# Performance work log

Hardware: AMD Instinct MI355X
Metric: run time of the kernel (lower is better)

Reference implementation:

```python
import jax, jax.numpy as jnp
import numpy as np
from functools import partial

N_NODES = 50000
N_EDGES = 800000
IN_F, HID_F, OUT_F = 128, 128, 64


def _linear_params(key, in_f, out_f):
    k1, k2 = jax.random.split(key)
    bound = 1.0 / np.sqrt(in_f)
    W = jax.random.uniform(k1, (out_f, in_f), jnp.float32, -bound, bound)
    b = jax.random.uniform(k2, (out_f,), jnp.float32, -bound, bound)
    return W, b


def setup_inputs() -> dict:
    key = jax.random.key(0)
    ks = jax.random.split(key, 10)
    features = jax.random.normal(ks[0], (N_NODES, IN_F), jnp.float32)
    src = jax.random.randint(ks[1], (N_EDGES,), 0, N_NODES, jnp.int32)
    dst = jax.random.randint(ks[2], (N_EDGES,), 0, N_NODES, jnp.int32)
    W1a, b1a = _linear_params(ks[3], IN_F, HID_F)
    W1b, b1b = _linear_params(ks[4], HID_F, HID_F)
    W2a, b2a = _linear_params(ks[5], HID_F, HID_F)
    W2b, b2b = _linear_params(ks[6], HID_F, HID_F)
    W3a, b3a = _linear_params(ks[7], HID_F, HID_F)
    W3b, b3b = _linear_params(ks[8], HID_F, OUT_F)
    return dict(features=features, src=src, dst=dst,
                W1a=W1a, b1a=b1a, W1b=W1b, b1b=b1b,
                W2a=W2a, b2a=b2a, W2b=W2b, b2b=b2b,
                W3a=W3a, b3a=b3a, W3b=W3b, b3b=b3b)


def _mean_agg(x, src, dst, n_nodes):
    # gather src features, segment-sum into dst, divide by in-degree (0-deg -> 0)
    summed = jax.ops.segment_sum(x[src], dst, num_segments=n_nodes)
    deg = jax.ops.segment_sum(jnp.ones((src.shape[0],), x.dtype), dst,
                              num_segments=n_nodes)
    return summed / jnp.maximum(deg, 1.0)[:, None]


def _gin_conv(x, src, dst, Wa, ba, Wb, bb):
    # DGL GINConv, aggregator 'mean', eps=0: h = MLP((1+eps)*x + mean_agg)
    h = x + _mean_agg(x, src, dst, x.shape[0])
    h = jax.nn.relu(h @ Wa.T + ba)
    return h @ Wb.T + bb


def reference(features, src, dst,
              W1a, b1a, W1b, b1b,
              W2a, b2a, W2b, b2b,
              W3a, b3a, W3b, b3b):
    x = jax.nn.relu(_gin_conv(features, src, dst, W1a, b1a, W1b, b1b))
    x = jax.nn.relu(_gin_conv(x, src, dst, W2a, b2a, W2b, b2b))
    x = jax.nn.relu(x @ W3a.T + b3a)
    return x @ W3b.T + b3b
```

## Files before the change

kernel.cpp:

```cpp
#include <hip/hip_runtime.h>
#include <hip/hip_fp16.h>

#define N_NODES 50000
#define N_EDGES 800000

typedef __attribute__((ext_vector_type(8))) short bf16x8;
typedef __attribute__((ext_vector_type(4))) float f32x4;

#define OFF_BUFA   0UL
#define OFF_T16    25600000UL
#define OFF_CNT    38400000UL
#define OFF_W      38600064UL
#define OFF_CSR    38960512UL

#define NB_EDGE 3125
#define NB_W    352
#define NB_FEAT 6250

__device__ __forceinline__ unsigned short bf16_rne(float f) {
  unsigned u = __float_as_uint(f);
  unsigned r = (u + 0x7FFFu + ((u >> 16) & 1u)) >> 16;
  return (unsigned short)r;
}

__device__ __forceinline__ int swz(int row, int b) {
  return (row * 256 + b) ^ ((row & 7) << 4);
}

__device__ __forceinline__ void gload_lds16(const void* g, void* l) {
  __builtin_amdgcn_global_load_lds(
      (const __attribute__((address_space(1))) unsigned int*)g,
      (__attribute__((address_space(3))) unsigned int*)l, 16, 0, 0);
}

__global__ __launch_bounds__(256)
void scatter16(const int* __restrict__ src, const int* __restrict__ dst,
               int* __restrict__ cnt, unsigned short* __restrict__ csr) {
  int i = blockIdx.x * 256 + threadIdx.x;
  int d = dst[i];
  int pos = atomicAdd(&cnt[d], 1);
  if (pos < 64) csr[(d << 6) + pos] = (unsigned short)src[i];
}

__global__ __launch_bounds__(256)
void conv_kernel(const float* __restrict__ W1a, const float* __restrict__ W1b,
                 const float* __restrict__ W2a, const float* __restrict__ W2b,
                 const float* __restrict__ W3a, const float* __restrict__ W3b,
                 unsigned short* __restrict__ pool,
                 const float* __restrict__ feat, __half* __restrict__ t16) {
  const int b = blockIdx.x;
  const int tid = threadIdx.x;
  if (b < NB_W) {
    int i = b * 256 + tid;
    const float* s;
    int base, local, msize;
    if (i < 16384)      { s = W1a; base = 0;      local = i;          msize = 16384; }
    else if (i < 32768) { s = W1b; base = 32768;  local = i - 16384;  msize = 16384; }
    else if (i < 49152) { s = W2a; base = 65536;  local = i - 32768;  msize = 16384; }
    else if (i < 65536) { s = W2b; base = 98304;  local = i - 49152;  msize = 16384; }
    else if (i < 81920) { s = W3a; base = 131072; local = i - 65536;  msize = 16384; }
    else                { s = W3b; base = 163840; local = i - 81920;  msize = 8192;  }
    float f = s[local];
    unsigned short hi = bf16_rne(f);
    float fh = __uint_as_float((unsigned)hi << 16);
    pool[base + local] = hi;
    pool[base + msize + local] = bf16_rne(f - fh);
  } else {
    int i = (b - NB_W) * 1024 + tid * 4;
    float4 v = *reinterpret_cast<const float4*>(feat + i);
    ushort4 h;
    h.x = __half_as_ushort(__float2half_rn(v.x));
    h.y = __half_as_ushort(__float2half_rn(v.y));
    h.z = __half_as_ushort(__float2half_rn(v.z));
    h.w = __half_as_ushort(__float2half_rn(v.w));
    *reinterpret_cast<ushort4*>((unsigned short*)t16 + i) = h;
  }
}

template <bool SELF32>
__global__ __launch_bounds__(256)
void agg_kernel(const __half* __restrict__ t16, const float* __restrict__ xself,
                const unsigned short* __restrict__ csr, const int* __restrict__ cnt,
                float* __restrict__ out) {
  int node = blockIdx.x * 4 + (threadIdx.x >> 6);
  if (node >= N_NODES) return;
  const int lane = threadIdx.x & 63;
  int deg = cnt[node];
  int dloop = min(deg, 64);
  int beg = node << 6;
  float inv = 1.0f / fmaxf((float)deg, 1.0f);

  float s0 = 0.f, s1 = 0.f, t0 = 0.f, t1 = 0.f;
  float u0 = 0.f, u1 = 0.f, v0 = 0.f, v1 = 0.f;
  int e = 0;
  for (; e + 3 < dloop; e += 4) {
    ushort4 q = *reinterpret_cast<const ushort4*>(csr + beg + e);
    float2 a = __half22float2(*reinterpret_cast<const __half2*>(t16 + (size_t)q.x * 128 + lane * 2));
    float2 b = __half22float2(*reinterpret_cast<const __half2*>(t16 + (size_t)q.y * 128 + lane * 2));
    float2 c = __half22float2(*reinterpret_cast<const __half2*>(t16 + (size_t)q.z * 128 + lane * 2));
    float2 d = __half22float2(*reinterpret_cast<const __half2*>(t16 + (size_t)q.w * 128 + lane * 2));
    s0 += a.x; s1 += a.y; t0 += b.x; t1 += b.y;
    u0 += c.x; u1 += c.y; v0 += d.x; v1 += d.y;
  }
  for (; e < dloop; ++e) {
    int i0 = csr[beg + e];
    float2 a = __half22float2(*reinterpret_cast<const __half2*>(t16 + (size_t)i0 * 128 + lane * 2));
    s0 += a.x; s1 += a.y;
  }
  float2 sm = make_float2(s0 + t0 + u0 + v0, s1 + t1 + u1 + v1);
  float2 xv;
  if (SELF32) {
    xv = *reinterpret_cast<const float2*>(xself + (size_t)node * 128 + lane * 2);
  } else {
    xv = __half22float2(*reinterpret_cast<const __half2*>(t16 + (size_t)node * 128 + lane * 2));
  }
  float2 o = make_float2(fmaf(sm.x, inv, xv.x), fmaf(sm.y, inv, xv.y));
  *reinterpret_cast<float2*>(out + (size_t)node * 128 + lane * 2) = o;
}

__device__ __forceinline__ void stage_x32(const float* __restrict__ X, int m0, int tid,
                                          char* ahi, char* alo, int M) {
  #pragma unroll
  for (int it = 0; it < 4; ++it) {
    int f = tid + it * 256;
    int row = f >> 5, c = f & 31;
    float4 v = make_float4(0.f, 0.f, 0.f, 0.f);
    if (m0 + row < M)
      v = *reinterpret_cast<const float4*>(X + (size_t)(m0 + row) * 128 + c * 4);
    ushort4 hi, lo;
    float fh;
    hi.x = bf16_rne(v.x); fh = __uint_as_float((unsigned)hi.x << 16); lo.x = bf16_rne(v.x - fh);
    hi.y = bf16_rne(v.y); fh = __uint_as_float((unsigned)hi.y << 16); lo.y = bf16_rne(v.y - fh);
    hi.z = bf16_rne(v.z); fh = __uint_as_float((unsigned)hi.z << 16); lo.z = bf16_rne(v.z - fh);
    hi.w = bf16_rne(v.w); fh = __uint_as_float((unsigned)hi.w << 16); lo.w = bf16_rne(v.w - fh);
    int bo = swz(row, c * 8);
    *reinterpret_cast<ushort4*>(ahi + bo) = hi;
    *reinterpret_cast<ushort4*>(alo + bo) = lo;
  }
}

template <int NR>
__device__ __forceinline__ void stage_w(const unsigned short* __restrict__ gh,
                                        const unsigned short* __restrict__ gl,
                                        char* WH, char* WL, int w, int lane) {
  constexpr int CH = NR / 16;
  #pragma unroll
  for (int k = 0; k < CH; ++k) {
    int base = w * (NR * 64) + k * 1024;
    int ofs = base + lane * 16;
    int row = ofs >> 8;
    int g = ofs ^ ((row & 7) << 4);
    gload_lds16((const char*)gh + g, WH + base);
    gload_lds16((const char*)gl + g, WL + base);
  }
}

template <int NB>
__device__ __forceinline__ void gemm_ll(const char* ahi, const char* alo,
                                        const char* wh, const char* wl,
                                        int w, int lrow, int lg,
                                        f32x4 (&acc)[2][NB]) {
  #pragma unroll
  for (int i = 0; i < 2; ++i)
    #pragma unroll
    for (int nb = 0; nb < NB; ++nb) acc[i][nb] = (f32x4){0.f, 0.f, 0.f, 0.f};
  #pragma unroll
  for (int kk = 0; kk < 4; ++kk) {
    bf16x8 bh[NB], bl[NB];
    #pragma unroll
    for (int nb = 0; nb < NB; ++nb) {
      int col = w * (16 * NB) + nb * 16 + lrow;
      int wo = swz(col, kk * 64 + lg * 16);
      bh[nb] = *reinterpret_cast<const bf16x8*>(wh + wo);
      bl[nb] = *reinterpret_cast<const bf16x8*>(wl + wo);
    }
    #pragma unroll
    for (int i = 0; i < 2; ++i) {
      int bo = swz(i * 16 + lrow, kk * 64 + lg * 16);
      bf16x8 ah = *reinterpret_cast<const bf16x8*>(ahi + bo);
      bf16x8 al = *reinterpret_cast<const bf16x8*>(alo + bo);
      #pragma unroll
      for (int nb = 0; nb < NB; ++nb) {
        acc[i][nb] = __builtin_amdgcn_mfma_f32_16x16x32_bf16(ah, bh[nb], acc[i][nb], 0, 0, 0);
        acc[i][nb] = __builtin_amdgcn_mfma_f32_16x16x32_bf16(al, bh[nb], acc[i][nb], 0, 0, 0);
        acc[i][nb] = __builtin_amdgcn_mfma_f32_16x16x32_bf16(ah, bl[nb], acc[i][nb], 0, 0, 0);
      }
    }
  }
}

__device__ __forceinline__ void store_h32(char* ahi, char* alo, const float* __restrict__ bias,
                                          int w, int lrow, int lg, f32x4 (&acc)[2][2]) {
  #pragma unroll
  for (int i = 0; i < 2; ++i) {
    #pragma unroll
    for (int nb = 0; nb < 2; ++nb) {
      int col = w * 32 + nb * 16 + lrow;
      float b = bias[col];
      #pragma unroll
      for (int r = 0; r < 4; ++r) {
        float v = fmaxf(acc[i][nb][r] + b, 0.f);
        int row = i * 16 + lg * 4 + r;
        unsigned short h = bf16_rne(v);
        float fh = __uint_as_float((unsigned)h << 16);
        unsigned short l2 = bf16_rne(v - fh);
        int bo = swz(row, col * 2);
        *reinterpret_cast<unsigned short*>(ahi + bo) = h;
        *reinterpret_cast<unsigned short*>(alo + bo) = l2;
      }
    }
  }
}

__global__ __launch_bounds__(256)
void mlp1_kernel(const float* __restrict__ X, const unsigned short* __restrict__ p,
                 const float* __restrict__ b1a, const float* __restrict__ b1b,
                 __half* __restrict__ Y, int M) {
  __shared__ __align__(16) unsigned short Ahi[32 * 128];
  __shared__ __align__(16) unsigned short Alo[32 * 128];
  __shared__ __align__(16) unsigned short WHs[128 * 128];
  __shared__ __align__(16) unsigned short WLs[128 * 128];
  char* ahi = (char*)Ahi;
  char* alo = (char*)Alo;
  char* wh = (char*)WHs;
  char* wl = (char*)WLs;
  const int tid = threadIdx.x;
  const int w = tid >> 6, l = tid & 63;
  const int lrow = l & 15, lg = l >> 4;
  const int m0 = blockIdx.x * 32;

  stage_w<128>(p + 0, p + 16384, wh, wl, w, l);
  stage_x32(X, m0, tid, ahi, alo, M);
  __syncthreads();

  f32x4 acc[2][2];
  gemm_ll<2>(ahi, alo, wh, wl, w, lrow, lg, acc);
  __syncthreads();

  stage_w<128>(p + 32768, p + 49152, wh, wl, w, l);
  store_h32(ahi, alo, b1a, w, lrow, lg, acc);
  __syncthreads();

  gemm_ll<2>(ahi, alo, wh, wl, w, lrow, lg, acc);

  #pragma unroll
  for (int i = 0; i < 2; ++i) {
    #pragma unroll
    for (int nb = 0; nb < 2; ++nb) {
      int col = w * 32 + nb * 16 + lrow;
      float b = b1b[col];
      #pragma unroll
      for (int r = 0; r < 4; ++r) {
        float v = fmaxf(acc[i][nb][r] + b, 0.f);
        int row = m0 + i * 16 + lg * 4 + r;
        if (row < M) Y[(size_t)row * 128 + col] = __float2half_rn(v);
      }
    }
  }
}

__global__ __launch_bounds__(256)
void mlp2head_kernel(const float* __restrict__ X, const unsigned short* __restrict__ p,
                     const float* __restrict__ b2a, const float* __restrict__ b2b,
                     const float* __restrict__ b3a, const float* __restrict__ b3b,
                     float* __restrict__ Y, int M) {
  __shared__ __align__(16) unsigned short Ahi[32 * 128];
  __shared__ __align__(16) unsigned short Alo[32 * 128];
  __shared__ __align__(16) unsigned short WHs[128 * 128];
  __shared__ __align__(16) unsigned short WLs[128 * 128];
  char* ahi = (char*)Ahi;
  char* alo = (char*)Alo;
  char* wh = (char*)WHs;
  char* wl = (char*)WLs;
  const int tid = threadIdx.x;
  const int w = tid >> 6, l = tid & 63;
  const int lrow = l & 15, lg = l >> 4;
  const int m0 = blockIdx.x * 32;

  stage_w<128>(p + 65536, p + 81920, wh, wl, w, l);
  stage_x32(X, m0, tid, ahi, alo, M);
  __syncthreads();

  f32x4 acc[2][2];
  gemm_ll<2>(ahi, alo, wh, wl, w, lrow, lg, acc);
  __syncthreads();

  stage_w<128>(p + 98304, p + 114688, wh, wl, w, l);
  store_h32(ahi, alo, b2a, w, lrow, lg, acc);
  __syncthreads();

  gemm_ll<2>(ahi, alo, wh, wl, w, lrow, lg, acc);
  __syncthreads();

  stage_w<128>(p + 131072, p + 147456, wh, wl, w, l);
  store_h32(ahi, alo, b2b, w, lrow, lg, acc);
  __syncthreads();

  gemm_ll<2>(ahi, alo, wh, wl, w, lrow, lg, acc);
  __syncthreads();

  stage_w<64>(p + 163840, p + 172032, wh, wl, w, l);
  store_h32(ahi, alo, b3a, w, lrow, lg, acc);
  __syncthreads();

  f32x4 acc1[2][1];
  gemm_ll<1>(ahi, alo, wh, wl, w, lrow, lg, acc1);

  #pragma unroll
  for (int i = 0; i < 2; ++i) {
    int col = w * 16 + lrow;
    float b = b3b[col];
    #pragma unroll
    for (int r = 0; r < 4; ++r) {
      float v = acc1[i][0][r] + b;
      int row = m0 + i * 16 + lg * 4 + r;
      if (row < M) Y[(size_t)row * 64 + col] = v;
    }
  }
}

extern "C" void kernel_launch(void* const* d_in, const int* in_sizes, int n_in,
                              void* d_out, int out_size, void* d_ws, size_t ws_size,
                              hipStream_t stream) {
  const float* feat = (const float*)d_in[0];
  const int*   esrc = (const int*)d_in[1];
  const int*   edst = (const int*)d_in[2];
  const float* W1a = (const float*)d_in[3];  const float* b1a = (const float*)d_in[4];
  const float* W1b = (const float*)d_in[5];  const float* b1b = (const float*)d_in[6];
  const float* W2a = (const float*)d_in[7];  const float* b2a = (const float*)d_in[8];
  const float* W2b = (const float*)d_in[9];  const float* b2b = (const float*)d_in[10];
  const float* W3a = (const float*)d_in[11]; const float* b3a = (const float*)d_in[12];
  const float* W3b = (const float*)d_in[13]; const float* b3b = (const float*)d_in[14];

  char* ws = (char*)d_ws;
  float*  bufA = (float*)(ws + OFF_BUFA);
  __half* t16  = (__half*)(ws + OFF_T16);
  int*    cnt  = (int*)(ws + OFF_CNT);
  unsigned short* p   = (unsigned short*)(ws + OFF_W);
  unsigned short* csr = (unsigned short*)(ws + OFF_CSR);

  hipMemsetAsync(cnt, 0, 200000, stream);

  scatter16<<<NB_EDGE, 256, 0, stream>>>(esrc, edst, cnt, csr);
  conv_kernel<<<NB_W + NB_FEAT, 256, 0, stream>>>(W1a, W1b, W2a, W2b, W3a, W3b, p, feat, t16);

  const int AB = (N_NODES + 3) / 4;
  const int GB = (N_NODES + 31) / 32;

  agg_kernel<true><<<AB, 256, 0, stream>>>(t16, feat, csr, cnt, bufA);
  mlp1_kernel<<<GB, 256, 0, stream>>>(bufA, p, b1a, b1b, t16, N_NODES);

  agg_kernel<false><<<AB, 256, 0, stream>>>(t16, feat, csr, cnt, bufA);
  mlp2head_kernel<<<GB, 256, 0, stream>>>(bufA, p, b2a, b2b, b3a, b3b,
                                          (float*)d_out, N_NODES);
}
```

Baseline: 211.5 us.

## Retile MLP kernels to 160-row blocks with 512 threads

Both fused MLP kernels move from 32-row tiles on 256 threads to 160-row tiles on 512 threads. Each of the 8 waves now owns a 16-column slice and loops over 10 row sub-tiles, reusing one weight fragment across them. The point is to amortize the per-block staging of the hi/lo bf16 weight matrices over five times as many rows, cutting weight traffic and block count. In exchange the much larger LDS footprint likely allows only one block per CU, and 313 blocks leave an uneven tail across the CUs.

```diff
diff --git a/kernel.cpp b/kernel.cpp
--- a/kernel.cpp
+++ b/kernel.cpp
@@ -16,6 +16,9 @@
 #define NB_EDGE 3125
 #define NB_W    352
 #define NB_FEAT 6250
+
+#define BM 160
+#define GB_MLP 313
 
 __device__ __forceinline__ unsigned short bf16_rne(float f) {
   unsigned u = __float_as_uint(f);
@@ -118,11 +121,11 @@
   *reinterpret_cast<float2*>(out + (size_t)node * 128 + lane * 2) = o;
 }
 
-__device__ __forceinline__ void stage_x32(const float* __restrict__ X, int m0, int tid,
-                                          char* ahi, char* alo, int M) {
-  #pragma unroll
-  for (int it = 0; it < 4; ++it) {
-    int f = tid + it * 256;
+__device__ __forceinline__ void stage_xT(const float* __restrict__ X, int m0, int tid,
+                                         char* ahi, char* alo, int M) {
+  #pragma unroll
+  for (int it = 0; it < 10; ++it) {
+    int f = tid + it * 512;
     int row = f >> 5, c = f & 31;
     float4 v = make_float4(0.f, 0.f, 0.f, 0.f);
     if (m0 + row < M)
@@ -143,10 +146,10 @@
 __device__ __forceinline__ void stage_w(const unsigned short* __restrict__ gh,
                                         const unsigned short* __restrict__ gl,
                                         char* WH, char* WL, int w, int lane) {
-  constexpr int CH = NR / 16;
+  constexpr int CH = NR / 32;
   #pragma unroll
   for (int k = 0; k < CH; ++k) {
-    int base = w * (NR * 64) + k * 1024;
+    int base = w * (NR * 32) + k * 1024;
     int ofs = base + lane * 16;
     int row = ofs >> 8;
     int g = ofs ^ ((row & 7) << 4);
@@ -155,166 +158,146 @@
   }
 }
 
-template <int NB>
-__device__ __forceinline__ void gemm_ll(const char* ahi, const char* alo,
-                                        const char* wh, const char* wl,
-                                        int w, int lrow, int lg,
-                                        f32x4 (&acc)[2][NB]) {
-  #pragma unroll
-  for (int i = 0; i < 2; ++i)
+__device__ __forceinline__ void gemmT(const char* ahi, const char* alo,
+                                      const char* wh, const char* wl,
+                                      int w, int lrow, int lg, f32x4 (&acc)[10]) {
+  #pragma unroll
+  for (int i = 0; i < 10; ++i) acc[i] = (f32x4){0.f, 0.f, 0.f, 0.f};
+  const int col = w * 16 + lrow;
+  #pragma unroll
+  for (int kk = 0; kk < 4; ++kk) {
+    int wo = swz(col, kk * 64 + lg * 16);
+    bf16x8 bh = *reinterpret_cast<const bf16x8*>(wh + wo);
+    bf16x8 bl = *reinterpret_cast<const bf16x8*>(wl + wo);
     #pragma unroll
-    for (int nb = 0; nb < NB; ++nb) acc[i][nb] = (f32x4){0.f, 0.f, 0.f, 0.f};
-  #pragma unroll
-  for (int kk = 0; kk < 4; ++kk) {
-    bf16x8 bh[NB], bl[NB];
-    #pragma unroll
-    for (int nb = 0; nb < NB; ++nb) {
-      int col = w * (16 * NB) + nb * 16 + lrow;
-      int wo = swz(col, kk * 64 + lg * 16);
-      bh[nb] = *reinterpret_cast<const bf16x8*>(wh + wo);
-      bl[nb] = *reinterpret_cast<const bf16x8*>(wl + wo);
-    }
-    #pragma unroll
-    for (int i = 0; i < 2; ++i) {
+    for (int i = 0; i < 10; ++i) {
       int bo = swz(i * 16 + lrow, kk * 64 + lg * 16);
       bf16x8 ah = *reinterpret_cast<const bf16x8*>(ahi + bo);
       bf16x8 al = *reinterpret_cast<const bf16x8*>(alo + bo);
-      #pragma unroll
-      for (int nb = 0; nb < NB; ++nb) {
-        acc[i][nb] = __builtin_amdgcn_mfma_f32_16x16x32_bf16(ah, bh[nb], acc[i][nb], 0, 0, 0);
-        acc[i][nb] = __builtin_amdgcn_mfma_f32_16x16x32_bf16(al, bh[nb], acc[i][nb], 0, 0, 0);
-        acc[i][nb] = __builtin_amdgcn_mfma_f32_16x16x32_bf16(ah, bl[nb], acc[i][nb], 0, 0, 0);
-      }
+      acc[i] = __builtin_amdgcn_mfma_f32_16x16x32_bf16(ah, bh, acc[i], 0, 0, 0);
+      acc[i] = __builtin_amdgcn_mfma_f32_16x16x32_bf16(al, bh, acc[i], 0, 0, 0);
+      acc[i] = __builtin_amdgcn_mfma_f32_16x16x32_bf16(ah, bl, acc[i], 0, 0, 0);
     }
   }
 }
 
-__device__ __forceinline__ void store_h32(char* ahi, char* alo, const float* __restrict__ bias,
-                                          int w, int lrow, int lg, f32x4 (&acc)[2][2]) {
-  #pragma unroll
-  for (int i = 0; i < 2; ++i) {
+__device__ __forceinline__ void store_hT(char* ahi, char* alo, const float* __restrict__ bias,
+                                         int w, int lrow, int lg, f32x4 (&acc)[10]) {
+  const int col = w * 16 + lrow;
+  const float b = bias[col];
+  #pragma unroll
+  for (int i = 0; i < 10; ++i) {
     #pragma unroll
-    for (int nb = 0; nb < 2; ++nb) {
-      int col = w * 32 + nb * 16 + lrow;
-      float b = bias[col];
-      #pragma unroll
-      for (int r = 0; r < 4; ++r) {
-        float v = fmaxf(acc[i][nb][r] + b, 0.f);
-        int row = i * 16 + lg * 4 + r;
-        unsigned short h = bf16_rne(v);
-        float fh = __uint_as_float((unsigned)h << 16);
-        unsigned short l2 = bf16_rne(v - fh);
-        int bo = swz(row, col * 2);
-        *reinterpret_cast<unsigned short*>(ahi + bo) = h;
-        *reinterpret_cast<unsigned short*>(alo + bo) = l2;
-      }
+    for (int r = 0; r < 4; ++r) {
+      float v = fmaxf(acc[i][r] + b, 0.f);
+      int row = i * 16 + lg * 4 + r;
+      unsigned short h = bf16_rne(v);
+      float fh = __uint_as_float((unsigned)h << 16);
+      unsigned short l2 = bf16_rne(v - fh);
+      int bo = swz(row, col * 2);
+      *reinterpret_cast<unsigned short*>(ahi + bo) = h;
+      *reinterpret_cast<unsigned short*>(alo + bo) = l2;
     }
   }
 }
 
-__global__ __launch_bounds__(256)
+__global__ __launch_bounds__(512, 2)
 void mlp1_kernel(const float* __restrict__ X, const unsigned short* __restrict__ p,
                  const float* __restrict__ b1a, const float* __restrict__ b1b,
                  __half* __restrict__ Y, int M) {
-  __shared__ __align__(16) unsigned short Ahi[32 * 128];
-  __shared__ __align__(16) unsigned short Alo[32 * 128];
+  __shared__ __align__(16) unsigned short Ahi[160 * 128];
+  __shared__ __align__(16) unsigned short Alo[160 * 128];
   __shared__ __align__(16) unsigned short WHs[128 * 128];
   __shared__ __align__(16) unsigned short WLs[128 * 128];
-  char* ahi = (char*)Ahi;
-  char* alo = (char*)Alo;
-  char* wh = (char*)WHs;
-  char* wl = (char*)WLs;
+  char* ahi = (char*)Ahi; char* alo = (char*)Alo;
+  char* wh = (char*)WHs;  char* wl = (char*)WLs;
   const int tid = threadIdx.x;
   const int w = tid >> 6, l = tid & 63;
   const int lrow = l & 15, lg = l >> 4;
-  const int m0 = blockIdx.x * 32;
+  const int m0 = blockIdx.x * BM;
 
   stage_w<128>(p + 0, p + 16384, wh, wl, w, l);
-  stage_x32(X, m0, tid, ahi, alo, M);
-  __syncthreads();
-
-  f32x4 acc[2][2];
-  gemm_ll<2>(ahi, alo, wh, wl, w, lrow, lg, acc);
+  stage_xT(X, m0, tid, ahi, alo, M);
+  __syncthreads();
+
+  f32x4 acc[10];
+  gemmT(ahi, alo, wh, wl, w, lrow, lg, acc);
   __syncthreads();
 
   stage_w<128>(p + 32768, p + 49152, wh, wl, w, l);
-  store_h32(ahi, alo, b1a, w, lrow, lg, acc);
-  __syncthreads();
-
-  gemm_ll<2>(ahi, alo, wh, wl, w, lrow, lg, acc);
-
-  #pragma unroll
-  for (int i = 0; i < 2; ++i) {
+  store_hT(ahi, alo, b1a, w, lrow, lg, acc);
+  __syncthreads();
+
+  gemmT(ahi, alo, wh, wl, w, lrow, lg, acc);
+
+  const int col = w * 16 + lrow;
+  const float b = b1b[col];
+  #pragma unroll
+  for (int i = 0; i < 10; ++i) {
     #pragma unroll
-    for (int nb = 0; nb < 2; ++nb) {
-      int col = w * 32 + nb * 16 + lrow;
-      float b = b1b[col];
-      #pragma unroll
-      for (int r = 0; r < 4; ++r) {
-        float v = fmaxf(acc[i][nb][r] + b, 0.f);
-        int row = m0 + i * 16 + lg * 4 + r;
-        if (row < M) Y[(size_t)row * 128 + col] = __float2half_rn(v);
-      }
+    for (int r = 0; r < 4; ++r) {
+      float v = fmaxf(acc[i][r] + b, 0.f);
+      int row = m0 + i * 16 + lg * 4 + r;
+      if (row < M) Y[(size_t)row * 128 + col] = __float2half_rn(v);
     }
   }
 }
 
-__global__ __launch_bounds__(256)
+__global__ __launch_bounds__(512, 2)
 void mlp2head_kernel(const float* __restrict__ X, const unsigned short* __restrict__ p,
                      const float* __restrict__ b2a, const float* __restrict__ b2b,
                      const float* __restrict__ b3a, const float* __restrict__ b3b,
                      float* __restrict__ Y, int M) {
-  __shared__ __align__(16) unsigned short Ahi[32 * 128];
-  __shared__ __align__(16) unsigned short Alo[32 * 128];
+  __shared__ __align__(16) unsigned short Ahi[160 * 128];
+  __shared__ __align__(16) unsigned short Alo[160 * 128];
   __shared__ __align__(16) unsigned short WHs[128 * 128];
   __shared__ __align__(16) unsigned short WLs[128 * 128];
-  char* ahi = (char*)Ahi;
-  char* alo = (char*)Alo;
-  char* wh = (char*)WHs;
-  char* wl = (char*)WLs;
+  char* ahi = (char*)Ahi; char* alo = (char*)Alo;
+  char* wh = (char*)WHs;  char* wl = (char*)WLs;
   const int tid = threadIdx.x;
   const int w = tid >> 6, l = tid & 63;
   const int lrow = l & 15, lg = l >> 4;
-  const int m0 = blockIdx.x * 32;
+  const int m0 = blockIdx.x * BM;
 
   stage_w<128>(p + 65536, p + 81920, wh, wl, w, l);
-  stage_x32(X, m0, tid, ahi, alo, M);
-  __syncthreads();
-
-  f32x4 acc[2][2];
-  gemm_ll<2>(ahi, alo, wh, wl, w, lrow, lg, acc);
+  stage_xT(X, m0, tid, ahi, alo, M);
+  __syncthreads();
+
+  f32x4 acc[10];
+  gemmT(ahi, alo, wh, wl, w, lrow, lg, acc);
   __syncthreads();
 
   stage_w<128>(p + 98304, p + 114688, wh, wl, w, l);
-  store_h32(ahi, alo, b2a, w, lrow, lg, acc);
-  __syncthreads();
-
-  gemm_ll<2>(ahi, alo, wh, wl, w, lrow, lg, acc);
+  store_hT(ahi, alo, b2a, w, lrow, lg, acc);
+  __syncthreads();
+
+  gemmT(ahi, alo, wh, wl, w, lrow, lg, acc);
   __syncthreads();
 
   stage_w<128>(p + 131072, p + 147456, wh, wl, w, l);
-  store_h32(ahi, alo, b2b, w, lrow, lg, acc);
-  __syncthreads();
-
-  gemm_ll<2>(ahi, alo, wh, wl, w, lrow, lg, acc);
+  store_hT(ahi, alo, b2b, w, lrow, lg, acc);
+  __syncthreads();
+
+  gemmT(ahi, alo, wh, wl, w, lrow, lg, acc);
   __syncthreads();
 
   stage_w<64>(p + 163840, p + 172032, wh, wl, w, l);
-  store_h32(ahi, alo, b3a, w, lrow, lg, acc);
-  __syncthreads();
-
-  f32x4 acc1[2][1];
-  gemm_ll<1>(ahi, alo, wh, wl, w, lrow, lg, acc1);
-
-  #pragma unroll
-  for (int i = 0; i < 2; ++i) {
-    int col = w * 16 + lrow;
-    float b = b3b[col];
+  store_hT(ahi, alo, b3a, w, lrow, lg, acc);
+  __syncthreads();
+
+  if (w < 4) {
+    f32x4 acc2[10];
+    gemmT(ahi, alo, wh, wl, w, lrow, lg, acc2);
+    const int col = w * 16 + lrow;
+    const float b = b3b[col];
     #pragma unroll
-    for (int r = 0; r < 4; ++r) {
-      float v = acc1[i][0][r] + b;
-      int row = m0 + i * 16 + lg * 4 + r;
-      if (row < M) Y[(size_t)row * 64 + col] = v;
+    for (int i = 0; i < 10; ++i) {
+      #pragma unroll
+      for (int r = 0; r < 4; ++r) {
+        float v = acc2[i][r] + b;
+        int row = m0 + i * 16 + lg * 4 + r;
+        if (row < M) Y[(size_t)row * 64 + col] = v;
+      }
     }
   }
 }
@@ -345,12 +328,11 @@
   conv_kernel<<<NB_W + NB_FEAT, 256, 0, stream>>>(W1a, W1b, W2a, W2b, W3a, W3b, p, feat, t16);
 
   const int AB = (N_NODES + 3) / 4;
-  const int GB = (N_NODES + 31) / 32;
 
   agg_kernel<true><<<AB, 256, 0, stream>>>(t16, feat, csr, cnt, bufA);
-  mlp1_kernel<<<GB, 256, 0, stream>>>(bufA, p, b1a, b1b, t16, N_NODES);
+  mlp1_kernel<<<GB_MLP, 512, 0, stream>>>(bufA, p, b1a, b1b, t16, N_NODES);
 
   agg_kernel<false><<<AB, 256, 0, stream>>>(t16, feat, csr, cnt, bufA);
-  mlp2head_kernel<<<GB, 256, 0, stream>>>(bufA, p, b2a, b2b, b3a, b3b,
-                                          (float*)d_out, N_NODES);
-}
+  mlp2head_kernel<<<GB_MLP, 512, 0, stream>>>(bufA, p, b2a, b2b, b3a, b3b,
+                                              (float*)d_out, N_NODES);
+}
```

New measurement: 234.7 us. 1.11x slower.
